# Kernel tuning notes

Hardware: AMD Instinct MI355X
Metric: run time of the kernel (lower is better)

Reference implementation:

```python
import jax, jax.numpy as jnp
import numpy as np

TINY = 1e-6  # TINY_NUMBER in the source repo
H, W, S = 256, 512, 64
N = H * W

def _unit(x, axis=-1):
    return x / jnp.maximum(jnp.linalg.norm(x, axis=axis, keepdims=True), 1e-4)

def setup_inputs() -> dict:
    key = jax.random.key(0)
    ks = jax.random.split(key, 9)
    normal = _unit(jax.random.normal(ks[0], (H, W, 3), jnp.float32))
    albedo = jax.random.uniform(ks[1], (H, W, 3), jnp.float32)
    roughness = jax.random.uniform(ks[2], (H, W, 1), jnp.float32)
    points = jax.random.normal(ks[3], (H, W, 3), jnp.float32)
    cam_position = jax.random.normal(ks[4], (3,), jnp.float32)
    light_dir_diff = _unit(jax.random.normal(ks[5], (N, S, 3), jnp.float32))
    diffuse_lighting = jax.random.uniform(ks[6], (N, S, 3), jnp.float32)
    h_dir_specular = _unit(jax.random.normal(ks[7], (N, S, 3), jnp.float32))
    specular_lighting = jax.random.uniform(ks[8], (N, S, 3), jnp.float32)
    return {"normal": normal, "albedo": albedo, "roughness": roughness,
            "points": points, "cam_position": cam_position,
            "light_dir_diff": light_dir_diff, "diffuse_lighting": diffuse_lighting,
            "h_dir_specular": h_dir_specular, "specular_lighting": specular_lighting}

def reference(normal, albedo, roughness, points, cam_position,
              light_dir_diff, diffuse_lighting, h_dir_specular, specular_lighting):
    env_h, env_w, _ = normal.shape
    n = normal.reshape(-1, 3)        # [N,3]
    a = albedo.reshape(-1, 3)        # [N,3]
    r = roughness.reshape(-1, 1)     # [N,1]
    p = points.reshape(-1, 3)        # [N,3]
    # view = F.normalize(cam - p, eps=1e-4): x / clamp(||x||, min=eps)
    d = cam_position[None, :] - p
    view = d / jnp.maximum(jnp.linalg.norm(d, axis=-1, keepdims=True), 1e-4)  # [N,3]

    def cdot(x, y):  # clamped dot over last axis, keepdim -> [...,1]
        return jnp.clip(jnp.sum(x * y, axis=-1, keepdims=True), 0.0, 1.0)

    # ---- diffuse: sum_s L * (albedo/pi) * ndl * 2*pi / S ----
    ndl_d = cdot(n[:, None, :], light_dir_diff)                      # [N,S,1]
    diffuse = jnp.sum(diffuse_lighting * (a[:, None, :] / np.pi) * ndl_d
                      * (2.0 * np.pi), axis=1) / S                   # [N,3]

    # ---- specular: GGX-style split-sum with importance-sampled half vectors ----
    v = view[:, None, :]                                             # [N,1,3]
    h = h_dir_specular                                               # [N,S,3]
    vdh = cdot(h, v)                                                 # [N,S,1]
    l_spec = 2.0 * vdh * h - v                                       # [N,S,3]
    ndl = cdot(n[:, None, :], l_spec)                                # [N,S,1]
    ndh = cdot(n[:, None, :], h)                                     # [N,S,1]
    ndv = cdot(n, view)[:, None, :]                                  # [N,1,1]
    f = 0.04 + 0.96 * jnp.exp2((-5.55472 * vdh - 6.98316) * vdh)     # Fresnel approx
    k = (r[:, None, :] + 1.0) ** 2 / 8.0                             # [N,1,1]
    g1_ndv = ndv / jnp.maximum(ndv * (1.0 - k) + k, TINY)
    g1_ndl = ndl / jnp.maximum(ndl * (1.0 - k) + k, TINY)
    brdf = f * (g1_ndl * g1_ndv) / jnp.maximum(4.0 * ndl * ndv, TINY)
    specular = jnp.sum(specular_lighting * brdf * ndl * 4.0 * vdh
                       / jnp.maximum(ndh, TINY), axis=1) / S         # [N,3]

    return (diffuse + specular).reshape(env_h, env_w, 3)
```

## Files before the change

kernel.cpp:

```cpp
#include <hip/hip_runtime.h>

#define TINY 1e-6f

constexpr int S_SAMPLES = 64;
constexpr int N_PIX = 256 * 512;

__device__ __forceinline__ float clamp01(float x) {
    return fminf(fmaxf(x, 0.0f), 1.0f);
}

__global__ void __launch_bounds__(256)
shade_kernel(const float* __restrict__ normal,
             const float* __restrict__ albedo,
             const float* __restrict__ roughness,
             const float* __restrict__ points,
             const float* __restrict__ cam,
             const float* __restrict__ ldir,
             const float* __restrict__ dlight,
             const float* __restrict__ hdir,
             const float* __restrict__ slight,
             float* __restrict__ out)
{
    const int wave = threadIdx.x >> 6;
    const int lane = threadIdx.x & 63;
    const int pix  = blockIdx.x * 4 + wave;

    const float nx = normal[pix * 3 + 0];
    const float ny = normal[pix * 3 + 1];
    const float nz = normal[pix * 3 + 2];
    const float r  = roughness[pix];
    const float px = points[pix * 3 + 0];
    const float py = points[pix * 3 + 1];
    const float pz = points[pix * 3 + 2];
    const float cx = cam[0], cy = cam[1], cz = cam[2];

    const float dx = cx - px, dy = cy - py, dz = cz - pz;
    const float len = sqrtf(dx * dx + dy * dy + dz * dz);
    const float inv = 1.0f / fmaxf(len, 1e-4f);
    const float vx = dx * inv, vy = dy * inv, vz = dz * inv;

    const float ndv = clamp01(nx * vx + ny * vy + nz * vz);
    const float k   = (r + 1.0f) * (r + 1.0f) * 0.125f;
    const float omk = 1.0f - k;
    const float g1v = ndv / fmaxf(ndv * omk + k, TINY);

    const long base = ((long)pix * S_SAMPLES + lane) * 3;

    const float lx = ldir[base + 0], ly = ldir[base + 1], lz = ldir[base + 2];
    const float d0 = dlight[base + 0], d1 = dlight[base + 1], d2 = dlight[base + 2];
    const float hx = hdir[base + 0], hy = hdir[base + 1], hz = hdir[base + 2];
    const float s0 = slight[base + 0], s1 = slight[base + 1], s2 = slight[base + 2];

    const float ndl_d = clamp01(nx * lx + ny * ly + nz * lz);
    float dacc0 = d0 * ndl_d;
    float dacc1 = d1 * ndl_d;
    float dacc2 = d2 * ndl_d;

    const float vdh = clamp01(hx * vx + hy * vy + hz * vz);
    const float tv  = 2.0f * vdh;
    const float lsx = tv * hx - vx;
    const float lsy = tv * hy - vy;
    const float lsz = tv * hz - vz;
    const float ndl = clamp01(nx * lsx + ny * lsy + nz * lsz);
    const float ndh = clamp01(nx * hx + ny * hy + nz * hz);
    const float f   = 0.04f + 0.96f * exp2f((-5.55472f * vdh - 6.98316f) * vdh);
    const float g1l = ndl / fmaxf(ndl * omk + k, TINY);
    const float brdf = f * (g1l * g1v) / fmaxf(4.0f * ndl * ndv, TINY);
    const float w    = brdf * ndl * 4.0f * vdh / fmaxf(ndh, TINY);
    float sacc0 = s0 * w;
    float sacc1 = s1 * w;
    float sacc2 = s2 * w;

#pragma unroll
    for (int off = 1; off < 64; off <<= 1) {
        dacc0 += __shfl_xor(dacc0, off);
        dacc1 += __shfl_xor(dacc1, off);
        dacc2 += __shfl_xor(dacc2, off);
        sacc0 += __shfl_xor(sacc0, off);
        sacc1 += __shfl_xor(sacc1, off);
        sacc2 += __shfl_xor(sacc2, off);
    }

    if (lane == 0) {
        const float ax = albedo[pix * 3 + 0];
        const float ay = albedo[pix * 3 + 1];
        const float az = albedo[pix * 3 + 2];
        const float inv_s = 1.0f / (float)S_SAMPLES;
        out[pix * 3 + 0] = (dacc0 * ax * 2.0f + sacc0) * inv_s;
        out[pix * 3 + 1] = (dacc1 * ay * 2.0f + sacc1) * inv_s;
        out[pix * 3 + 2] = (dacc2 * az * 2.0f + sacc2) * inv_s;
    }
}

extern "C" void kernel_launch(void* const* d_in, const int* in_sizes, int n_in,
                              void* d_out, int out_size, void* d_ws, size_t ws_size,
                              hipStream_t stream) {
    const float* normal    = (const float*)d_in[0];
    const float* albedo    = (const float*)d_in[1];
    const float* roughness = (const float*)d_in[2];
    const float* points    = (const float*)d_in[3];
    const float* cam       = (const float*)d_in[4];
    const float* ldir      = (const float*)d_in[5];
    const float* dlight    = (const float*)d_in[6];
    const float* hdir      = (const float*)d_in[7];
    const float* slight    = (const float*)d_in[8];
    float* out = (float*)d_out;

    const int blocks = N_PIX / 4;
    shade_kernel<<<blocks, 256, 0, stream>>>(normal, albedo, roughness, points,
                                             cam, ldir, dlight, hdir, slight, out);
}
```

Measured before the change: 348.2 us.

## Vectorize sample loads with float4 and process four samples per thread

Each thread now handles four samples of a pixel, loading its 48 contiguous bytes from each per-sample array as three float4 loads, and 16 threads share a pixel instead of 64. This cuts load instruction count, shortens the cross-lane shuffle reduction, and amortizes per-pixel setup across more samples. Divisions are also replaced with the hardware approximate reciprocal, which slightly changes numerical accuracy.

```diff
diff --git a/kernel.cpp b/kernel.cpp
--- a/kernel.cpp
+++ b/kernel.cpp
@@ -2,11 +2,22 @@
 
 #define TINY 1e-6f
 
-constexpr int S_SAMPLES = 64;
 constexpr int N_PIX = 256 * 512;
 
 __device__ __forceinline__ float clamp01(float x) {
     return fminf(fmaxf(x, 0.0f), 1.0f);
+}
+
+__device__ __forceinline__ float frcp(float x) {
+    return __builtin_amdgcn_rcpf(x);
+}
+
+__device__ __forceinline__ float cget(const float4& a, const float4& b, const float4& c, int i) {
+    switch (i) {
+        case 0:  return a.x; case 1:  return a.y; case 2:  return a.z; case 3:  return a.w;
+        case 4:  return b.x; case 5:  return b.y; case 6:  return b.z; case 7:  return b.w;
+        case 8:  return c.x; case 9:  return c.y; case 10: return c.z; default: return c.w;
+    }
 }
 
 __global__ void __launch_bounds__(256)
@@ -21,9 +32,20 @@
              const float* __restrict__ slight,
              float* __restrict__ out)
 {
-    const int wave = threadIdx.x >> 6;
-    const int lane = threadIdx.x & 63;
-    const int pix  = blockIdx.x * 4 + wave;
+    const int t   = threadIdx.x;
+    const int grp = t >> 4;
+    const int sub = t & 15;
+    const int pix = blockIdx.x * 16 + grp;
+
+    const size_t fbase = (size_t)pix * 192 + (size_t)sub * 12;
+    const float4* Lp = (const float4*)(ldir   + fbase);
+    const float4* Dp = (const float4*)(dlight + fbase);
+    const float4* Hp = (const float4*)(hdir   + fbase);
+    const float4* Sp = (const float4*)(slight + fbase);
+    const float4 L0 = Lp[0], L1 = Lp[1], L2 = Lp[2];
+    const float4 D0 = Dp[0], D1 = Dp[1], D2 = Dp[2];
+    const float4 H0 = Hp[0], H1 = Hp[1], H2 = Hp[2];
+    const float4 S0 = Sp[0], S1 = Sp[1], S2 = Sp[2];
 
     const float nx = normal[pix * 3 + 0];
     const float ny = normal[pix * 3 + 1];
@@ -36,43 +58,56 @@
 
     const float dx = cx - px, dy = cy - py, dz = cz - pz;
     const float len = sqrtf(dx * dx + dy * dy + dz * dz);
-    const float inv = 1.0f / fmaxf(len, 1e-4f);
+    const float inv = frcp(fmaxf(len, 1e-4f));
     const float vx = dx * inv, vy = dy * inv, vz = dz * inv;
 
     const float ndv = clamp01(nx * vx + ny * vy + nz * vz);
     const float k   = (r + 1.0f) * (r + 1.0f) * 0.125f;
     const float omk = 1.0f - k;
-    const float g1v = ndv / fmaxf(ndv * omk + k, TINY);
+    const float g1v = ndv * frcp(fmaxf(ndv * omk + k, TINY));
 
-    const long base = ((long)pix * S_SAMPLES + lane) * 3;
-
-    const float lx = ldir[base + 0], ly = ldir[base + 1], lz = ldir[base + 2];
-    const float d0 = dlight[base + 0], d1 = dlight[base + 1], d2 = dlight[base + 2];
-    const float hx = hdir[base + 0], hy = hdir[base + 1], hz = hdir[base + 2];
-    const float s0 = slight[base + 0], s1 = slight[base + 1], s2 = slight[base + 2];
-
-    const float ndl_d = clamp01(nx * lx + ny * ly + nz * lz);
-    float dacc0 = d0 * ndl_d;
-    float dacc1 = d1 * ndl_d;
-    float dacc2 = d2 * ndl_d;
-
-    const float vdh = clamp01(hx * vx + hy * vy + hz * vz);
-    const float tv  = 2.0f * vdh;
-    const float lsx = tv * hx - vx;
-    const float lsy = tv * hy - vy;
-    const float lsz = tv * hz - vz;
-    const float ndl = clamp01(nx * lsx + ny * lsy + nz * lsz);
-    const float ndh = clamp01(nx * hx + ny * hy + nz * hz);
-    const float f   = 0.04f + 0.96f * exp2f((-5.55472f * vdh - 6.98316f) * vdh);
-    const float g1l = ndl / fmaxf(ndl * omk + k, TINY);
-    const float brdf = f * (g1l * g1v) / fmaxf(4.0f * ndl * ndv, TINY);
-    const float w    = brdf * ndl * 4.0f * vdh / fmaxf(ndh, TINY);
-    float sacc0 = s0 * w;
-    float sacc1 = s1 * w;
-    float sacc2 = s2 * w;
+    float dacc0 = 0.f, dacc1 = 0.f, dacc2 = 0.f;
+    float sacc0 = 0.f, sacc1 = 0.f, sacc2 = 0.f;
 
 #pragma unroll
-    for (int off = 1; off < 64; off <<= 1) {
+    for (int j = 0; j < 4; ++j) {
+        const int e = j * 3;
+        const float lx = cget(L0, L1, L2, e + 0);
+        const float ly = cget(L0, L1, L2, e + 1);
+        const float lz = cget(L0, L1, L2, e + 2);
+        const float d0 = cget(D0, D1, D2, e + 0);
+        const float d1 = cget(D0, D1, D2, e + 1);
+        const float d2 = cget(D0, D1, D2, e + 2);
+        const float hx = cget(H0, H1, H2, e + 0);
+        const float hy = cget(H0, H1, H2, e + 1);
+        const float hz = cget(H0, H1, H2, e + 2);
+        const float s0 = cget(S0, S1, S2, e + 0);
+        const float s1 = cget(S0, S1, S2, e + 1);
+        const float s2 = cget(S0, S1, S2, e + 2);
+
+        const float ndl_d = clamp01(nx * lx + ny * ly + nz * lz);
+        dacc0 += d0 * ndl_d;
+        dacc1 += d1 * ndl_d;
+        dacc2 += d2 * ndl_d;
+
+        const float vdh = clamp01(hx * vx + hy * vy + hz * vz);
+        const float tv  = 2.0f * vdh;
+        const float lsx = tv * hx - vx;
+        const float lsy = tv * hy - vy;
+        const float lsz = tv * hz - vz;
+        const float ndl = clamp01(nx * lsx + ny * lsy + nz * lsz);
+        const float ndh = clamp01(nx * hx + ny * hy + nz * hz);
+        const float f   = 0.04f + 0.96f * exp2f((-5.55472f * vdh - 6.98316f) * vdh);
+        const float g1l = ndl * frcp(fmaxf(ndl * omk + k, TINY));
+        const float brdf = f * g1l * g1v * frcp(fmaxf(4.0f * ndl * ndv, TINY));
+        const float w    = brdf * ndl * 4.0f * vdh * frcp(fmaxf(ndh, TINY));
+        sacc0 += s0 * w;
+        sacc1 += s1 * w;
+        sacc2 += s2 * w;
+    }
+
+#pragma unroll
+    for (int off = 1; off < 16; off <<= 1) {
         dacc0 += __shfl_xor(dacc0, off);
         dacc1 += __shfl_xor(dacc1, off);
         dacc2 += __shfl_xor(dacc2, off);
@@ -81,11 +116,11 @@
         sacc2 += __shfl_xor(sacc2, off);
     }
 
-    if (lane == 0) {
+    if (sub == 0) {
         const float ax = albedo[pix * 3 + 0];
         const float ay = albedo[pix * 3 + 1];
         const float az = albedo[pix * 3 + 2];
-        const float inv_s = 1.0f / (float)S_SAMPLES;
+        const float inv_s = 1.0f / 64.0f;
         out[pix * 3 + 0] = (dacc0 * ax * 2.0f + sacc0) * inv_s;
         out[pix * 3 + 1] = (dacc1 * ay * 2.0f + sacc1) * inv_s;
         out[pix * 3 + 2] = (dacc2 * az * 2.0f + sacc2) * inv_s;
@@ -106,7 +141,7 @@
     const float* slight    = (const float*)d_in[8];
     float* out = (float*)d_out;
 
-    const int blocks = N_PIX / 4;
+    const int blocks = N_PIX / 16;
     shade_kernel<<<blocks, 256, 0, stream>>>(normal, albedo, roughness, points,
                                              cam, ldir, dlight, hdir, slight, out);
 }
```

New measurement: 344.9 us. Within noise of the previous version (-0.9%).
